# Optimization experiments

Hardware: AMD Instinct MI355X
Metric: run time of the kernel (lower is better)

The kernel has to match this reference:

```python
import jax, jax.numpy as jnp
from jax import lax
import numpy as np

D_MODEL, D_INNER, D_STATE, DT_RANK, D_CONV = 1024, 2048, 16, 64, 4
BATCH, SEQ = 2, 1024
EPS = 1e-5


def setup_inputs() -> dict:
    key = jax.random.key(0)
    ks = jax.random.split(key, 10)
    s_in = 1.0 / np.sqrt(D_MODEL)
    s_x = 1.0 / np.sqrt(D_INNER)
    s_dt = DT_RANK ** -0.5
    # dt_proj bias init as in the source: inv-softplus of dt ~ logU(1e-3, 1e-1)
    dt = jnp.exp(jax.random.uniform(ks[7], (D_INNER,)) * (np.log(0.1) - np.log(0.001)) + np.log(0.001))
    dt = jnp.clip(dt, 1e-4, None)
    inv_dt = dt + jnp.log(-jnp.expm1(-dt))
    A_log = jnp.log(jnp.broadcast_to(jnp.arange(1, D_STATE + 1, dtype=jnp.float32), (D_INNER, D_STATE)))
    return {
        "u": jax.random.normal(ks[0], (BATCH, SEQ, D_MODEL), jnp.float32),
        "w_norm": jnp.ones((D_MODEL,), jnp.float32),
        "w_in": jax.random.normal(ks[1], (2 * D_INNER, D_MODEL), jnp.float32) * s_in,
        "conv_w": jax.random.normal(ks[2], (D_INNER, 1, D_CONV), jnp.float32) * 0.5,
        "conv_b": jax.random.normal(ks[3], (D_INNER,), jnp.float32) * 0.1,
        "w_x": jax.random.normal(ks[4], (DT_RANK + 2 * D_STATE, D_INNER), jnp.float32) * s_x,
        "w_dt": jax.random.uniform(ks[5], (D_INNER, DT_RANK), jnp.float32, -s_dt, s_dt),
        "b_dt": inv_dt,
        "A_log": A_log,
        "D_param": jnp.ones((D_INNER,), jnp.float32),
        "w_out": jax.random.normal(ks[6], (D_MODEL, D_INNER), jnp.float32) * s_x,
    }


def reference(u, w_norm, w_in, conv_w, conv_b, w_x, w_dt, b_dt, A_log, D_param, w_out):
    d_inner, d_state = A_log.shape
    dt_rank = w_dt.shape[1]
    # RMSNorm
    rms = jnp.sqrt(jnp.mean(u * u, axis=-1, keepdims=True) + EPS)
    u_norm = w_norm * (u / rms)
    # in_proj -> split x, z
    xz = jnp.einsum('bld,ed->ble', u_norm, w_in)
    x, z = jnp.split(xz, 2, axis=-1)
    # causal depthwise conv1d (left pad d_conv-1 == torch pad+truncate)
    xt = x.transpose(0, 2, 1)  # (B, D, L)
    conv = lax.conv_general_dilated(
        xt, conv_w, window_strides=(1,), padding=[(conv_w.shape[-1] - 1, 0)],
        feature_group_count=d_inner, dimension_numbers=('NCH', 'OIH', 'NCH'))
    x = jax.nn.silu((conv + conv_b[None, :, None]).transpose(0, 2, 1))  # (B, L, D)
    # x_proj -> dt, B, C
    xp = jnp.einsum('bld,ed->ble', x, w_x)
    dt_r = xp[..., :dt_rank]
    Bm = xp[..., dt_rank:dt_rank + d_state]   # (B, L, N)
    Cm = xp[..., dt_rank + d_state:]          # (B, L, N)
    dt = jax.nn.softplus(jnp.einsum('blr,dr->bld', dt_r, w_dt) + b_dt)
    # discretize
    A = -jnp.exp(A_log)                        # (D, N)
    dA = jnp.exp(dt[..., None] * A)            # (B, L, D, N)
    dBu = dt[..., None] * Bm[:, :, None, :] * x[..., None]  # (B, L, D, N)
    # sequential selective scan over L via lax.scan
    def step(s, inp):
        dA_t, dBu_t, C_t = inp
        s = dA_t * s + dBu_t                   # (B, D, N)
        y_t = jnp.einsum('bdn,bn->bd', s, C_t)
        return s, y_t
    s0 = jnp.zeros((u.shape[0], d_inner, d_state), x.dtype)
    _, ys = lax.scan(step, s0, (dA.transpose(1, 0, 2, 3), dBu.transpose(1, 0, 2, 3), Cm.transpose(1, 0, 2)))
    y = ys.transpose(1, 0, 2) + x * D_param    # (B, L, D)
    # gate + out_proj + residual
    y = y * jax.nn.silu(z)
    return jnp.einsum('bld,ed->ble', y, w_out) + u
```

## Files before the change

### kernel.cpp

```cpp
#include <hip/hip_runtime.h>
#include <hip/hip_bf16.h>
#include <cstdint>
#include <cstddef>

#define D_MODEL 1024
#define D_INNER 2048
#define D_STATE 16
#define DT_RANK 64
#define D_CONV  4
#define BATCH   2
#define SEQ     1024
#define NTOK    (BATCH*SEQ)
#define NC      32
#define CHUNK   (SEQ/NC)

typedef __bf16 bf16;
typedef __attribute__((ext_vector_type(8))) __bf16 bf16x8;
typedef __attribute__((ext_vector_type(4))) float f32x4;

#define WS_UNORM   0
#define WS_WIN     (WS_UNORM + 4194304)
#define WS_WOUT    (WS_WIN + 8388608)
#define WS_WX      (WS_WOUT + 4194304)
#define WS_XZB     (WS_WX + 524288)
#define WS_XCB     (WS_XZB + 16777216)
#define WS_XP      (WS_XCB + 8388608)
#define WS_DT      (WS_XP + 1048576)
#define WS_P       (WS_DT + 16777216)
#define WS_Q       (WS_P + 8388608)
#define WS_S       (WS_Q + 8388608)
#define WS_YB      (WS_S + 8388608)

__device__ __forceinline__ void gload16(const void* gsrc, void* ldst) {
    __builtin_amdgcn_global_load_lds(
        (const __attribute__((address_space(1))) unsigned int*)gsrc,
        (__attribute__((address_space(3))) unsigned int*)ldst,
        16, 0, 0);
}

__global__ void mamba_prep(const float* __restrict__ u, const float* __restrict__ w_norm,
                           const float* __restrict__ w_in, const float* __restrict__ w_x,
                           const float* __restrict__ w_out,
                           bf16* __restrict__ unorm, bf16* __restrict__ winb,
                           bf16* __restrict__ wxb, bf16* __restrict__ woutb,
                           float* __restrict__ outp, float* __restrict__ xp) {
    __shared__ float red[4];
    int bid = blockIdx.x, tid = threadIdx.x;
    if (bid < 2048) {
        int t = bid;
        const float4 v = ((const float4*)(u + (size_t)t * D_MODEL))[tid];
        float ss = v.x * v.x + v.y * v.y + v.z * v.z + v.w * v.w;
        #pragma unroll
        for (int off = 32; off; off >>= 1) ss += __shfl_xor(ss, off, 64);
        int lane = tid & 63, wv = tid >> 6;
        if (lane == 0) red[wv] = ss;
        __syncthreads();
        float tot = red[0] + red[1] + red[2] + red[3];
        float rinv = rsqrtf(tot * (1.0f / D_MODEL) + 1e-5f);
        const float4 wn = ((const float4*)w_norm)[tid];
        bf16* op = unorm + (size_t)t * D_MODEL + tid * 4;
        op[0] = (bf16)(v.x * wn.x * rinv);
        op[1] = (bf16)(v.y * wn.y * rinv);
        op[2] = (bf16)(v.z * wn.z * rinv);
        op[3] = (bf16)(v.w * wn.w * rinv);
    } else if (bid < 6144) {
        int i = (bid - 2048) * 256 + tid;
        float4 v = ((const float4*)w_in)[i];
        bf16* o = winb + i * 4;
        o[0] = (bf16)v.x; o[1] = (bf16)v.y; o[2] = (bf16)v.z; o[3] = (bf16)v.w;
    } else if (bid < 8192) {
        int i = (bid - 6144) * 256 + tid;
        float4 v = ((const float4*)w_out)[i];
        bf16* o = woutb + i * 4;
        o[0] = (bf16)v.x; o[1] = (bf16)v.y; o[2] = (bf16)v.z; o[3] = (bf16)v.w;
    } else if (bid < 8448) {
        int i = (bid - 8192) * 256 + tid;
        bf16* o = wxb + i * 4;
        if (i < 49152) {
            float4 v = ((const float4*)w_x)[i];
            o[0] = (bf16)v.x; o[1] = (bf16)v.y; o[2] = (bf16)v.z; o[3] = (bf16)v.w;
        } else {
            o[0] = (bf16)0.f; o[1] = (bf16)0.f; o[2] = (bf16)0.f; o[3] = (bf16)0.f;
        }
    } else if (bid < 10496) {
        int i = (bid - 8448) * 256 + tid;
        ((float4*)outp)[i] = ((const float4*)u)[i];
    } else {
        int i = (bid - 10496) * 256 + tid;
        ((float4*)xp)[i] = (float4){0.f, 0.f, 0.f, 0.f};
    }
}

template <int EPI, int SPLITK>
__global__ __launch_bounds__(256)
void mamba_gemm(const bf16* __restrict__ A, const bf16* __restrict__ B, void* __restrict__ Cv,
                int M, int N, int K) {
    __shared__ __align__(16) bf16 As[128 * 64];
    __shared__ __align__(16) bf16 Bs[128 * 64];
    int tid = threadIdx.x;
    int lane = tid & 63, w = tid >> 6;
    int wr = w >> 1, wc = w & 1;
    int m0 = blockIdx.y * 128, n0 = blockIdx.x * 128;
    int r16 = lane & 15, kq = lane >> 4;

    int Kc = K / SPLITK;
    int kbeg = blockIdx.z * Kc;
    int kend = kbeg + Kc;

    f32x4 acc[4][4];
    #pragma unroll
    for (int i = 0; i < 4; ++i)
        #pragma unroll
        for (int j = 0; j < 4; ++j)
            acc[i][j] = (f32x4){0.f, 0.f, 0.f, 0.f};

    int srow = tid >> 3;
    int p    = tid & 7;

    for (int k0 = kbeg; k0 < kend; k0 += 64) {
        __syncthreads();
        #pragma unroll
        for (int s = 0; s < 4; ++s) {
            int row = s * 32 + srow;
            int q = p ^ (row & 7);
            gload16(A + (size_t)(m0 + row) * K + k0 + q * 8,
                    (char*)As + s * 4096 + w * 1024);
            gload16(B + (size_t)(n0 + row) * K + k0 + q * 8,
                    (char*)Bs + s * 4096 + w * 1024);
        }
        __syncthreads();
        #pragma unroll
        for (int sub = 0; sub < 2; ++sub) {
            bf16x8 af[4], bfr[4];
            #pragma unroll
            for (int i = 0; i < 4; ++i) {
                int ra = wr * 64 + i * 16 + r16;
                int slot = (sub * 4 + kq) ^ (ra & 7);
                af[i] = *(const bf16x8*)((const char*)As + ra * 128 + slot * 16);
            }
            #pragma unroll
            for (int j = 0; j < 4; ++j) {
                int rb = wc * 64 + j * 16 + r16;
                int slot = (sub * 4 + kq) ^ (rb & 7);
                bfr[j] = *(const bf16x8*)((const char*)Bs + rb * 128 + slot * 16);
            }
            #pragma unroll
            for (int i = 0; i < 4; ++i)
                #pragma unroll
                for (int j = 0; j < 4; ++j)
                    acc[i][j] = __builtin_amdgcn_mfma_f32_16x16x32_bf16(af[i], bfr[j], acc[i][j], 0, 0, 0);
        }
    }

    #pragma unroll
    for (int i = 0; i < 4; ++i)
        #pragma unroll
        for (int j = 0; j < 4; ++j) {
            int col = n0 + wc * 64 + j * 16 + r16;
            #pragma unroll
            for (int r = 0; r < 4; ++r) {
                int row = m0 + wr * 64 + i * 16 + kq * 4 + r;
                float v = acc[i][j][r];
                size_t idx = (size_t)row * N + col;
                if (EPI == 2) {
                    atomicAdd(&((float*)Cv)[idx], v);
                } else {
                    ((bf16*)Cv)[idx] = (bf16)v;
                }
            }
        }
}

__global__ __launch_bounds__(256)
void mamba_dtgemm(const float* __restrict__ xp, const float* __restrict__ wdt,
                  const float* __restrict__ bdt, float* __restrict__ dt) {
    __shared__ __align__(16) bf16 As[128 * 64];
    __shared__ __align__(16) bf16 Bs[128 * 64];
    int tid = threadIdx.x;
    int lane = tid & 63, w = tid >> 6;
    int wr = w >> 1, wc = w & 1;
    int m0 = blockIdx.y * 128, n0 = blockIdx.x * 128;
    int r16 = lane & 15, kq = lane >> 4;

    #pragma unroll
    for (int s4 = 0; s4 < 4; ++s4) {
        int s = s4 * 256 + tid;
        int row = s >> 3, p = s & 7;
        int ps = p ^ (row & 7);
        const float* ga = xp + (size_t)(m0 + row) * 128 + p * 8;
        const float* gb = wdt + (size_t)(n0 + row) * 64 + p * 8;
        float4 a0 = *(const float4*)ga, a1 = *(const float4*)(ga + 4);
        float4 b0 = *(const float4*)gb, b1 = *(const float4*)(gb + 4);
        bf16x8 av, bv;
        av[0] = (bf16)a0.x; av[1] = (bf16)a0.y; av[2] = (bf16)a0.z; av[3] = (bf16)a0.w;
        av[4] = (bf16)a1.x; av[5] = (bf16)a1.y; av[6] = (bf16)a1.z; av[7] = (bf16)a1.w;
        bv[0] = (bf16)b0.x; bv[1] = (bf16)b0.y; bv[2] = (bf16)b0.z; bv[3] = (bf16)b0.w;
        bv[4] = (bf16)b1.x; bv[5] = (bf16)b1.y; bv[6] = (bf16)b1.z; bv[7] = (bf16)b1.w;
        *(bf16x8*)((char*)As + row * 128 + ps * 16) = av;
        *(bf16x8*)((char*)Bs + row * 128 + ps * 16) = bv;
    }
    __syncthreads();

    f32x4 acc[4][4];
    #pragma unroll
    for (int i = 0; i < 4; ++i)
        #pragma unroll
        for (int j = 0; j < 4; ++j)
            acc[i][j] = (f32x4){0.f, 0.f, 0.f, 0.f};

    #pragma unroll
    for (int sub = 0; sub < 2; ++sub) {
        bf16x8 af[4], bfr[4];
        #pragma unroll
        for (int i = 0; i < 4; ++i) {
            int ra = wr * 64 + i * 16 + r16;
            int slot = (sub * 4 + kq) ^ (ra & 7);
            af[i] = *(const bf16x8*)((const char*)As + ra * 128 + slot * 16);
        }
        #pragma unroll
        for (int j = 0; j < 4; ++j) {
            int rb = wc * 64 + j * 16 + r16;
            int slot = (sub * 4 + kq) ^ (rb & 7);
            bfr[j] = *(const bf16x8*)((const char*)Bs + rb * 128 + slot * 16);
        }
        #pragma unroll
        for (int i = 0; i < 4; ++i)
            #pragma unroll
            for (int j = 0; j < 4; ++j)
                acc[i][j] = __builtin_amdgcn_mfma_f32_16x16x32_bf16(af[i], bfr[j], acc[i][j], 0, 0, 0);
    }

    #pragma unroll
    for (int i = 0; i < 4; ++i)
        #pragma unroll
        for (int j = 0; j < 4; ++j) {
            int col = n0 + wc * 64 + j * 16 + r16;
            float bias = bdt[col];
            #pragma unroll
            for (int r = 0; r < 4; ++r) {
                int row = m0 + wr * 64 + i * 16 + kq * 4 + r;
                float v = acc[i][j][r] + bias;
                v = (v > 20.f) ? v : log1pf(__expf(v));
                dt[(size_t)row * D_INNER + col] = v;
            }
        }
}

__global__ void mamba_conv(const bf16* __restrict__ xzb, const float* __restrict__ cw,
                           const float* __restrict__ cb, bf16* __restrict__ xcb) {
    int gid = blockIdx.x * 256 + threadIdx.x;
    int d = gid & (D_INNER - 1);
    int t = gid >> 11;
    int l = t & (SEQ - 1);
    int b = t >> 10;
    float4 wv = ((const float4*)cw)[d];
    const float wj[4] = {wv.x, wv.y, wv.z, wv.w};
    float acc = cb[d];
    #pragma unroll
    for (int j = 0; j < 4; ++j) {
        int li = l - 3 + j;
        if (li >= 0) acc += wj[j] * (float)xzb[(size_t)(b * SEQ + li) * 4096 + d];
    }
    float s = acc / (1.f + __expf(-acc));
    xcb[gid] = (bf16)s;
}

__global__ void mamba_scan1(const float* __restrict__ dt, const bf16* __restrict__ xcb,
                            const float* __restrict__ xp, const float* __restrict__ A_log,
                            float* __restrict__ P, float* __restrict__ Q) {
    int bid = blockIdx.x;
    int db = bid & 7, c = (bid >> 3) & 31, b = bid >> 8;
    int d = db * 256 + threadIdx.x;
    float a[D_STATE], pv[D_STATE], q[D_STATE];
    #pragma unroll
    for (int n = 0; n < D_STATE; ++n) {
        a[n] = -__expf(A_log[d * D_STATE + n]);
        pv[n] = 1.f; q[n] = 0.f;
    }
    int tbase = b * SEQ + c * CHUNK;
    for (int i = 0; i < CHUNK; ++i) {
        size_t t = tbase + i;
        float dtv = dt[t * D_INNER + d];
        float xv  = (float)xcb[t * D_INNER + d];
        float dtx = dtv * xv;
        const float* xpr = xp + t * 128;
        #pragma unroll
        for (int n = 0; n < D_STATE; ++n) {
            float e = __expf(dtv * a[n]);
            q[n] = e * q[n] + dtx * xpr[64 + n];
            pv[n] *= e;
        }
    }
    float* Pp = P + ((size_t)(b * D_INNER + d) * NC + c) * D_STATE;
    float* Qp = Q + ((size_t)(b * D_INNER + d) * NC + c) * D_STATE;
    #pragma unroll
    for (int n = 0; n < D_STATE; ++n) { Pp[n] = pv[n]; Qp[n] = q[n]; }
}

__global__ void mamba_scan2(const float* __restrict__ P, const float* __restrict__ Q,
                            float* __restrict__ S) {
    int gid = blockIdx.x * 256 + threadIdx.x;
    int bd = gid >> 4, n = gid & 15;
    size_t base = (size_t)bd * NC * D_STATE + n;
    float s = 0.f;
    for (int c = 0; c < NC; ++c) {
        S[base + c * D_STATE] = s;
        s = P[base + c * D_STATE] * s + Q[base + c * D_STATE];
    }
}

__global__ void mamba_scan3(const float* __restrict__ dt, const bf16* __restrict__ xcb,
                            const float* __restrict__ xp, const float* __restrict__ A_log,
                            const float* __restrict__ S, const float* __restrict__ Dp,
                            const bf16* __restrict__ xzb, bf16* __restrict__ yb) {
    int bid = blockIdx.x;
    int db = bid & 7, c = (bid >> 3) & 31, b = bid >> 8;
    int d = db * 256 + threadIdx.x;
    float a[D_STATE], s[D_STATE];
    const float* Sp = S + ((size_t)(b * D_INNER + d) * NC + c) * D_STATE;
    #pragma unroll
    for (int n = 0; n < D_STATE; ++n) {
        a[n] = -__expf(A_log[d * D_STATE + n]);
        s[n] = Sp[n];
    }
    float Dpd = Dp[d];
    int tbase = b * SEQ + c * CHUNK;
    for (int i = 0; i < CHUNK; ++i) {
        size_t t = tbase + i;
        float dtv = dt[t * D_INNER + d];
        float xv  = (float)xcb[t * D_INNER + d];
        float dtx = dtv * xv;
        const float* xpr = xp + t * 128;
        float y = 0.f;
        #pragma unroll
        for (int n = 0; n < D_STATE; ++n) {
            float e = __expf(dtv * a[n]);
            s[n] = e * s[n] + dtx * xpr[64 + n];
            y += s[n] * xpr[80 + n];
        }
        float zv = (float)xzb[t * 4096 + 2048 + d];
        float sig = 1.f / (1.f + __expf(-zv));
        float out = (y + xv * Dpd) * (zv * sig);
        yb[t * D_INNER + d] = (bf16)out;
    }
}

extern "C" void kernel_launch(void* const* d_in, const int* in_sizes, int n_in,
                              void* d_out, int out_size, void* d_ws, size_t ws_size,
                              hipStream_t stream) {
    const float* u      = (const float*)d_in[0];
    const float* w_norm = (const float*)d_in[1];
    const float* w_in   = (const float*)d_in[2];
    const float* conv_w = (const float*)d_in[3];
    const float* conv_b = (const float*)d_in[4];
    const float* w_x    = (const float*)d_in[5];
    const float* w_dt   = (const float*)d_in[6];
    const float* b_dt   = (const float*)d_in[7];
    const float* A_log  = (const float*)d_in[8];
    const float* D_par  = (const float*)d_in[9];
    const float* w_out  = (const float*)d_in[10];
    float* out = (float*)d_out;

    char* ws = (char*)d_ws;
    bf16* unorm = (bf16*)(ws + WS_UNORM);
    bf16* winb  = (bf16*)(ws + WS_WIN);
    bf16* woutb = (bf16*)(ws + WS_WOUT);
    bf16* wxb   = (bf16*)(ws + WS_WX);
    bf16* xzb   = (bf16*)(ws + WS_XZB);
    bf16* xcb   = (bf16*)(ws + WS_XCB);
    float* xp   = (float*)(ws + WS_XP);
    float* dtb  = (float*)(ws + WS_DT);
    float* Pb   = (float*)(ws + WS_P);
    float* Qb   = (float*)(ws + WS_Q);
    float* Sb   = (float*)(ws + WS_S);
    bf16* yb    = (bf16*)(ws + WS_YB);

    mamba_prep<<<10752, 256, 0, stream>>>(u, w_norm, w_in, w_x, w_out,
                                          unorm, winb, wxb, woutb, out, xp);

    mamba_gemm<3, 1><<<dim3(32, 16, 1), 256, 0, stream>>>(unorm, winb, xzb,
                                                          NTOK, 2 * D_INNER, D_MODEL);

    mamba_conv<<<NTOK * D_INNER / 256, 256, 0, stream>>>(xzb, conv_w, conv_b, xcb);

    mamba_gemm<2, 8><<<dim3(1, 16, 8), 256, 0, stream>>>(xcb, wxb, xp,
                                                         NTOK, 128, D_INNER);

    mamba_dtgemm<<<dim3(16, 16), 256, 0, stream>>>(xp, w_dt, b_dt, dtb);

    mamba_scan1<<<512, 256, 0, stream>>>(dtb, xcb, xp, A_log, Pb, Qb);
    mamba_scan2<<<256, 256, 0, stream>>>(Pb, Qb, Sb);
    mamba_scan3<<<512, 256, 0, stream>>>(dtb, xcb, xp, A_log, Sb, D_par, xzb, yb);

    mamba_gemm<2, 4><<<dim3(8, 16, 4), 256, 0, stream>>>(yb, woutb, out,
                                                         NTOK, D_MODEL, D_INNER);
}
```

Baseline: 273.9 us.

## Double-buffer GEMM LDS, remap blocks across XCDs, store dt as bf16

The bf16 GEMM now uses two LDS buffers, so the next K tile is staged while the current one is consumed. Block indices are remapped so consecutive logical tiles spread across the eight XCDs. dt is written and read as bf16 instead of fp32, which halves its memory traffic in the scan kernels. The x_proj split-K factor rises from 8 to 16. Costs include doubled LDS per block, possibly lower occupancy, more atomics, and reduced dt precision.

```diff
diff --git a/kernel.cpp b/kernel.cpp
--- a/kernel.cpp
+++ b/kernel.cpp
@@ -26,7 +26,7 @@
 #define WS_XCB     (WS_XZB + 16777216)
 #define WS_XP      (WS_XCB + 8388608)
 #define WS_DT      (WS_XP + 1048576)
-#define WS_P       (WS_DT + 16777216)
+#define WS_P       (WS_DT + 8388608)
 #define WS_Q       (WS_P + 8388608)
 #define WS_S       (WS_Q + 8388608)
 #define WS_YB      (WS_S + 8388608)
@@ -95,17 +95,26 @@
 __global__ __launch_bounds__(256)
 void mamba_gemm(const bf16* __restrict__ A, const bf16* __restrict__ B, void* __restrict__ Cv,
                 int M, int N, int K) {
-    __shared__ __align__(16) bf16 As[128 * 64];
-    __shared__ __align__(16) bf16 Bs[128 * 64];
+    __shared__ __align__(16) bf16 As[2][128 * 64];
+    __shared__ __align__(16) bf16 Bs[2][128 * 64];
     int tid = threadIdx.x;
     int lane = tid & 63, w = tid >> 6;
     int wr = w >> 1, wc = w & 1;
-    int m0 = blockIdx.y * 128, n0 = blockIdx.x * 128;
     int r16 = lane & 15, kq = lane >> 4;
 
+    int NXB = gridDim.x, NYB = gridDim.y;
+    int nwg = NXB * NYB * SPLITK;
+    int flat = blockIdx.x + NXB * (blockIdx.y + NYB * blockIdx.z);
+    int logical = (flat & 7) * (nwg >> 3) + (flat >> 3);
+    int by = logical % NYB;
+    int t2 = logical / NYB;
+    int bx = t2 % NXB;
+    int bz = t2 / NXB;
+
+    int m0 = by * 128, n0 = bx * 128;
     int Kc = K / SPLITK;
-    int kbeg = blockIdx.z * Kc;
-    int kend = kbeg + Kc;
+    int kbeg = bz * Kc;
+    int nt = Kc / 64;
 
     f32x4 acc[4][4];
     #pragma unroll
@@ -114,21 +123,26 @@
         for (int j = 0; j < 4; ++j)
             acc[i][j] = (f32x4){0.f, 0.f, 0.f, 0.f};
 
-    int srow = tid >> 3;
-    int p    = tid & 7;
-
-    for (int k0 = kbeg; k0 < kend; k0 += 64) {
-        __syncthreads();
+    const int srow = tid >> 3;
+    const int p    = tid & 7;
+
+    auto STAGE = [&](int buf, int k0) {
         #pragma unroll
         for (int s = 0; s < 4; ++s) {
             int row = s * 32 + srow;
             int q = p ^ (row & 7);
             gload16(A + (size_t)(m0 + row) * K + k0 + q * 8,
-                    (char*)As + s * 4096 + w * 1024);
+                    (char*)As[buf] + s * 4096 + w * 1024);
             gload16(B + (size_t)(n0 + row) * K + k0 + q * 8,
-                    (char*)Bs + s * 4096 + w * 1024);
-        }
+                    (char*)Bs[buf] + s * 4096 + w * 1024);
+        }
+    };
+
+    STAGE(0, kbeg);
+    for (int t = 0; t < nt; ++t) {
         __syncthreads();
+        if (t + 1 < nt) STAGE((t + 1) & 1, kbeg + (t + 1) * 64);
+        int cur = t & 1;
         #pragma unroll
         for (int sub = 0; sub < 2; ++sub) {
             bf16x8 af[4], bfr[4];
@@ -136,13 +150,13 @@
             for (int i = 0; i < 4; ++i) {
                 int ra = wr * 64 + i * 16 + r16;
                 int slot = (sub * 4 + kq) ^ (ra & 7);
-                af[i] = *(const bf16x8*)((const char*)As + ra * 128 + slot * 16);
+                af[i] = *(const bf16x8*)((const char*)As[cur] + ra * 128 + slot * 16);
             }
             #pragma unroll
             for (int j = 0; j < 4; ++j) {
                 int rb = wc * 64 + j * 16 + r16;
                 int slot = (sub * 4 + kq) ^ (rb & 7);
-                bfr[j] = *(const bf16x8*)((const char*)Bs + rb * 128 + slot * 16);
+                bfr[j] = *(const bf16x8*)((const char*)Bs[cur] + rb * 128 + slot * 16);
             }
             #pragma unroll
             for (int i = 0; i < 4; ++i)
@@ -173,7 +187,7 @@
 
 __global__ __launch_bounds__(256)
 void mamba_dtgemm(const float* __restrict__ xp, const float* __restrict__ wdt,
-                  const float* __restrict__ bdt, float* __restrict__ dt) {
+                  const float* __restrict__ bdt, bf16* __restrict__ dt) {
     __shared__ __align__(16) bf16 As[128 * 64];
     __shared__ __align__(16) bf16 Bs[128 * 64];
     int tid = threadIdx.x;
@@ -241,7 +255,7 @@
                 int row = m0 + wr * 64 + i * 16 + kq * 4 + r;
                 float v = acc[i][j][r] + bias;
                 v = (v > 20.f) ? v : log1pf(__expf(v));
-                dt[(size_t)row * D_INNER + col] = v;
+                dt[(size_t)row * D_INNER + col] = (bf16)v;
             }
         }
 }
@@ -265,7 +279,7 @@
     xcb[gid] = (bf16)s;
 }
 
-__global__ void mamba_scan1(const float* __restrict__ dt, const bf16* __restrict__ xcb,
+__global__ void mamba_scan1(const bf16* __restrict__ dt, const bf16* __restrict__ xcb,
                             const float* __restrict__ xp, const float* __restrict__ A_log,
                             float* __restrict__ P, float* __restrict__ Q) {
     int bid = blockIdx.x;
@@ -280,7 +294,7 @@
     int tbase = b * SEQ + c * CHUNK;
     for (int i = 0; i < CHUNK; ++i) {
         size_t t = tbase + i;
-        float dtv = dt[t * D_INNER + d];
+        float dtv = (float)dt[t * D_INNER + d];
         float xv  = (float)xcb[t * D_INNER + d];
         float dtx = dtv * xv;
         const float* xpr = xp + t * 128;
@@ -309,7 +323,7 @@
     }
 }
 
-__global__ void mamba_scan3(const float* __restrict__ dt, const bf16* __restrict__ xcb,
+__global__ void mamba_scan3(const bf16* __restrict__ dt, const bf16* __restrict__ xcb,
                             const float* __restrict__ xp, const float* __restrict__ A_log,
                             const float* __restrict__ S, const float* __restrict__ Dp,
                             const bf16* __restrict__ xzb, bf16* __restrict__ yb) {
@@ -327,7 +341,7 @@
     int tbase = b * SEQ + c * CHUNK;
     for (int i = 0; i < CHUNK; ++i) {
         size_t t = tbase + i;
-        float dtv = dt[t * D_INNER + d];
+        float dtv = (float)dt[t * D_INNER + d];
         float xv  = (float)xcb[t * D_INNER + d];
         float dtx = dtv * xv;
         const float* xpr = xp + t * 128;
@@ -369,7 +383,7 @@
     bf16* xzb   = (bf16*)(ws + WS_XZB);
     bf16* xcb   = (bf16*)(ws + WS_XCB);
     float* xp   = (float*)(ws + WS_XP);
-    float* dtb  = (float*)(ws + WS_DT);
+    bf16* dtb   = (bf16*)(ws + WS_DT);
     float* Pb   = (float*)(ws + WS_P);
     float* Qb   = (float*)(ws + WS_Q);
     float* Sb   = (float*)(ws + WS_S);
@@ -383,8 +397,8 @@
 
     mamba_conv<<<NTOK * D_INNER / 256, 256, 0, stream>>>(xzb, conv_w, conv_b, xcb);
 
-    mamba_gemm<2, 8><<<dim3(1, 16, 8), 256, 0, stream>>>(xcb, wxb, xp,
-                                                         NTOK, 128, D_INNER);
+    mamba_gemm<2, 16><<<dim3(1, 16, 16), 256, 0, stream>>>(xcb, wxb, xp,
+                                                           NTOK, 128, D_INNER);
 
     mamba_dtgemm<<<dim3(16, 16), 256, 0, stream>>>(xp, w_dt, b_dt, dtb);
 
```

Result: no change. 273.4 us (-0.2%).
